# Kernel optimization log

Measured on AMD Instinct MI355X. Metric: run time of the kernel, lower is better.

The kernel has to match this reference:

```python
import jax, jax.numpy as jnp
import numpy as np

N = 50000      # nodes
E = 1000000    # edges
D = 64         # hidden dim
F_IN = 19      # node feature dim (nfeat_node)
EH = 50        # edge attr dim (nc_edge_hidden)
B = 128        # graphs in batch
NB = 3         # n_block
CUTOFF = 5.0
LOG2 = 0.6931471805599453


def ssp(x):
    # shifted softplus, Act('ssp')
    return jax.nn.softplus(x) - LOG2


def setup_inputs() -> dict:
    key = jax.random.key(0)
    ks = iter(jax.random.split(key, 48))
    def nrm(shape, scale=0.05):
        return jax.random.normal(next(ks), shape, dtype=jnp.float32) * scale
    inp = {}
    inp['x'] = jax.random.normal(next(ks), (N, F_IN), dtype=jnp.float32)
    inp['edge_index'] = jax.random.randint(next(ks), (2, E), 0, N)
    inp['edge_weight'] = jax.random.uniform(next(ks), (E,), dtype=jnp.float32, minval=0.5, maxval=CUTOFF)
    inp['edge_attr'] = jax.random.normal(next(ks), (E, EH), dtype=jnp.float32)
    inp['z'] = jax.random.randint(next(ks), (N,), 0, 100)
    inp['batch'] = jnp.sort(jax.random.randint(next(ks), (N,), 0, B))
    inp['lin0_w'] = nrm((D, F_IN)); inp['lin0_b'] = nrm((D,))
    # 3 NNConv blocks, weights stacked on leading axis
    inp['conv_mlp_w1'] = nrm((NB, 32, EH)); inp['conv_mlp_b1'] = nrm((NB, 32))
    inp['conv_mlp_w2'] = nrm((NB, D, 32)); inp['conv_mlp_b2'] = nrm((NB, D))
    inp['conv_lin1_w'] = nrm((NB, D, D))
    inp['conv_lin2_w'] = nrm((NB, D, D)); inp['conv_lin2_b'] = nrm((NB, D))
    inp['conv_lin3_w'] = nrm((NB, D, D)); inp['conv_lin3_b'] = nrm((NB, D))
    inp['gru_w_ih'] = nrm((3 * D, D)); inp['gru_w_hh'] = nrm((3 * D, D))
    inp['gru_b_ih'] = nrm((3 * D,)); inp['gru_b_hh'] = nrm((3 * D,))
    # Set2Set LSTM: input 2*D, hidden D
    inp['lstm_w_ih'] = nrm((4 * D, 2 * D)); inp['lstm_w_hh'] = nrm((4 * D, D))
    inp['lstm_b_ih'] = nrm((4 * D,)); inp['lstm_b_hh'] = nrm((4 * D,))
    inp['lin1_w'] = nrm((D, 2 * D)); inp['lin1_b'] = nrm((D,))
    inp['lin2_w'] = nrm((1, D)); inp['lin2_b'] = nrm((1,))
    inp['atom_ref'] = nrm((100, 1)); inp['energy_ref'] = nrm((100, 1))
    return inp


def _forward(x, edge_weight, edge_attr, lin0_w, lin0_b,
             conv_mlp_w1, conv_mlp_b1, conv_mlp_w2, conv_mlp_b2,
             conv_lin1_w, conv_lin2_w, conv_lin2_b, conv_lin3_w, conv_lin3_b,
             gru_w_ih, gru_w_hh, gru_b_ih, gru_b_hh,
             lstm_w_ih, lstm_w_hh, lstm_b_ih, lstm_b_hh,
             lin1_w, lin1_b, lin2_w, lin2_b, atom_ref, energy_ref,
             edge_index, z, batch):
    src = edge_index[0]   # neighbor j (source)
    dst = edge_index[1]   # center i (target), aggr='mean'
    deg = jnp.clip(jax.ops.segment_sum(jnp.ones((E,), jnp.float32), dst, num_segments=N), 1.0, None)
    # cosine cutoff envelope
    C = jnp.cos(edge_weight * jnp.pi / CUTOFF) * 0.5 + 0.5  # (E,)
    out = jax.nn.leaky_relu(x @ lin0_w.T + lin0_b)  # (N, D)
    h = out
    for b in range(NB):
        # edge MLP: Linear(EH,32) -> ReLU -> Linear(32,D), scaled by envelope
        Wm = jax.nn.relu(edge_attr @ conv_mlp_w1[b].T + conv_mlp_b1[b]) @ conv_mlp_w2[b].T + conv_mlp_b2[b]
        Wm = Wm * C[:, None]  # (E, D)
        hx = out @ conv_lin1_w[b].T  # (N, D)
        msg = hx[src] * Wm  # gather + per-edge product  (E, D)
        agg = jax.ops.segment_sum(msg, dst, num_segments=N) / deg[:, None]  # mean aggregation
        m = ssp(agg @ conv_lin2_w[b].T + conv_lin2_b[b]) @ conv_lin3_w[b].T + conv_lin3_b[b]
        # GRU node-state update (single step)
        gi = m @ gru_w_ih.T + gru_b_ih
        gh = h @ gru_w_hh.T + gru_b_hh
        i_r, i_z, i_n = jnp.split(gi, 3, axis=-1)
        h_r, h_z, h_n = jnp.split(gh, 3, axis=-1)
        r = jax.nn.sigmoid(i_r + h_r)
        zg = jax.nn.sigmoid(i_z + h_z)
        n = jnp.tanh(i_n + r * h_n)
        h = (1.0 - zg) * n + zg * h
        out = h
    # Set2Set readout, processing_steps=3
    q_star = jnp.zeros((B, 2 * D), jnp.float32)
    hl = jnp.zeros((B, D), jnp.float32)
    cl = jnp.zeros((B, D), jnp.float32)
    for _ in range(3):
        gates = q_star @ lstm_w_ih.T + lstm_b_ih + hl @ lstm_w_hh.T + lstm_b_hh
        gi_, gf_, gg_, go_ = jnp.split(gates, 4, axis=-1)
        cl = jax.nn.sigmoid(gf_) * cl + jax.nn.sigmoid(gi_) * jnp.tanh(gg_)
        hl = jax.nn.sigmoid(go_) * jnp.tanh(cl)
        q = hl  # (B, D)
        e = jnp.sum(out * q[batch], axis=-1)  # (N,)
        emax = jax.ops.segment_max(e, batch, num_segments=B)
        a = jnp.exp(e - emax[batch])
        asum = jax.ops.segment_sum(a, batch, num_segments=B)
        a = a / asum[batch]  # per-graph softmax attention
        r_read = jax.ops.segment_sum(a[:, None] * out, batch, num_segments=B)
        q_star = jnp.concatenate([q, r_read], axis=-1)
    g = jax.nn.relu(q_star @ lin1_w.T + lin1_b)
    energy = g @ lin2_w.T + lin2_b  # (B, 1)
    ref = jax.ops.segment_sum((energy_ref[z] + atom_ref[z])[:, 0], batch, num_segments=B)
    return energy + ref[:, None]


def reference(x, edge_weight, edge_attr, lin0_w, lin0_b,
              conv_mlp_w1, conv_mlp_b1, conv_mlp_w2, conv_mlp_b2,
              conv_lin1_w, conv_lin2_w, conv_lin2_b, conv_lin3_w, conv_lin3_b,
              gru_w_ih, gru_w_hh, gru_b_ih, gru_b_hh,
              lstm_w_ih, lstm_w_hh, lstm_b_ih, lstm_b_hh,
              lin1_w, lin1_b, lin2_w, lin2_b, atom_ref, energy_ref,
              edge_index, z, batch):
    return _forward(x, edge_weight, edge_attr, lin0_w, lin0_b,
                    conv_mlp_w1, conv_mlp_b1, conv_mlp_w2, conv_mlp_b2,
                    conv_lin1_w, conv_lin2_w, conv_lin2_b, conv_lin3_w, conv_lin3_b,
                    gru_w_ih, gru_w_hh, gru_b_ih, gru_b_hh,
                    lstm_w_ih, lstm_w_hh, lstm_b_ih, lstm_b_hh,
                    lin1_w, lin1_b, lin2_w, lin2_b, atom_ref, energy_ref,
                    edge_index, z, batch)
```

## Files before the change

kernel.cpp:

```cpp
#include <hip/hip_runtime.h>
#include <math.h>

#define NN 50000
#define NE 1000000
#define D 64
#define FIN 19
#define EHD 50
#define NG 128
#define NBLK 3
#define NB1 196
#define EAPW 32

#define PI_OVER_CUT 0.6283185307179586f
#define LN2F 0.6931471805599453f

static __device__ __forceinline__ float sspf(float x) {
  return fmaxf(x, 0.0f) + log1pf(expf(-fabsf(x))) - LN2F;
}
static __device__ __forceinline__ float sigm(float x) {
  return 1.0f / (1.0f + expf(-x));
}

typedef _Float16 h2f __attribute__((ext_vector_type(2)));
typedef __fp16   p2f __attribute__((ext_vector_type(2)));
typedef unsigned int u32x4 __attribute__((ext_vector_type(4)));

static __device__ __forceinline__ unsigned int f16pair(float a, float b) {
  p2f r = __builtin_amdgcn_cvt_pkrtz(a, b);
  return __builtin_bit_cast(unsigned int, r);
}
static __device__ __forceinline__ float f16lo(unsigned int u) {
  h2f v = __builtin_bit_cast(h2f, u);
  return (float)v.x;
}
static __device__ __forceinline__ float f16hi(unsigned int u) {
  h2f v = __builtin_bit_cast(h2f, u);
  return (float)v.y;
}

#if __has_builtin(__builtin_amdgcn_fdot2)
static __device__ __forceinline__ float dot2(unsigned int a, unsigned int b, float c) {
  return __builtin_amdgcn_fdot2(__builtin_bit_cast(h2f, a),
                                __builtin_bit_cast(h2f, b), c, false);
}
#else
static __device__ __forceinline__ float dot2(unsigned int a, unsigned int b, float c) {
  h2f a2 = __builtin_bit_cast(h2f, a), b2 = __builtin_bit_cast(h2f, b);
  return c + (float)a2.x * (float)b2.x + (float)a2.y * (float)b2.y;
}
#endif

__global__ __launch_bounds__(256) void k_deg(const int* __restrict__ ei,
                                             int* __restrict__ degi) {
  int e = blockIdx.x * 256 + threadIdx.x;
  if (e < NE) atomicAdd(&degi[ei[NE + e]], 1);
}

__global__ __launch_bounds__(256) void k_scan1(int* __restrict__ degi,
                                               int* __restrict__ start,
                                               float* __restrict__ dinv,
                                               int* __restrict__ bsum) {
  __shared__ int sc[256];
  int t = threadIdx.x;
  int i = blockIdx.x * 256 + t;
  int d = (i < NN) ? degi[i] : 0;
  sc[t] = d; __syncthreads();
  for (int off = 1; off < 256; off <<= 1) {
    int u = (t >= off) ? sc[t - off] : 0;
    __syncthreads();
    sc[t] += u;
    __syncthreads();
  }
  if (i < NN) {
    start[i] = sc[t] - d;
    dinv[i] = 1.0f / fmaxf((float)d, 1.0f);
    degi[i] = 0;
  }
  if (t == 255) bsum[blockIdx.x] = sc[255];
}

__global__ __launch_bounds__(256) void k_scan2(int* __restrict__ bsum) {
  __shared__ int sc[256];
  int t = threadIdx.x;
  int v = (t < NB1) ? bsum[t] : 0;
  sc[t] = v; __syncthreads();
  for (int off = 1; off < 256; off <<= 1) {
    int u = (t >= off) ? sc[t - off] : 0;
    __syncthreads();
    sc[t] += u;
    __syncthreads();
  }
  bsum[t] = sc[t] - v;
}

__global__ __launch_bounds__(256) void k_scan3(int* __restrict__ start,
                                               const int* __restrict__ bsum) {
  int i = blockIdx.x * 256 + threadIdx.x;
  if (i < NN) start[i] += bsum[blockIdx.x];
  if (i == 0) start[NN] = NE;
}

template<int PACK>
__global__ __launch_bounds__(256) void k_slot2(const int* __restrict__ ei,
                                               const int* __restrict__ start,
                                               int* __restrict__ cursor,
                                               int* __restrict__ es,
                                               const float* __restrict__ ea,
                                               unsigned int* __restrict__ eap) {
  int e = blockIdx.x * 256 + threadIdx.x;
  if (e >= NE) return;
  int dst = ei[NE + e];
  int ofs = atomicAdd(&cursor[dst], 1);
  int s = start[dst] + ofs;
  es[s] = e;
  if (PACK) {
    const float2* er = (const float2*)(ea + (size_t)e * EHD);
    unsigned int tmp[25];
    #pragma unroll
    for (int k2 = 0; k2 < 25; k2++) {
      float2 v = er[k2];
      tmp[k2] = f16pair(v.x, v.y);
    }
    u32x4* op = (u32x4*)(eap + (size_t)s * EAPW);
    #pragma unroll
    for (int i = 0; i < 6; i++) {
      u32x4 v4 = {tmp[4*i], tmp[4*i+1], tmp[4*i+2], tmp[4*i+3]};
      __builtin_nontemporal_store(v4, op + i);
    }
    u32x4 v6 = {tmp[24], 0u, 0u, 0u};
    __builtin_nontemporal_store(v6, op + 6);
    u32x4 v7 = {0u, 0u, 0u, 0u};
    __builtin_nontemporal_store(v7, op + 7);
  }
}

__global__ __launch_bounds__(256) void k_fill(const int* __restrict__ es,
                                              const int* __restrict__ ei,
                                              const float* __restrict__ ew,
                                              int* __restrict__ ssrc,
                                              int* __restrict__ sdst,
                                              float* __restrict__ Cp) {
  int s = blockIdx.x * 256 + threadIdx.x;
  if (s >= NE) return;
  int e = es[s];
  ssrc[s] = ei[e];
  sdst[s] = ei[NE + e];
  Cp[s] = cosf(ew[e] * PI_OVER_CUT) * 0.5f + 0.5f;
}

__global__ __launch_bounds__(256) void k_wprep(const float* __restrict__ w1,
                                               const float* __restrict__ w2,
                                               const float* __restrict__ cl2w,
                                               const float* __restrict__ cl3w,
                                               const float* __restrict__ cl1w,
                                               const float* __restrict__ gwih,
                                               const float* __restrict__ gwhh,
                                               unsigned int* __restrict__ w1h,
                                               unsigned int* __restrict__ w2h,
                                               unsigned int* __restrict__ nl2h,
                                               unsigned int* __restrict__ nl3h,
                                               unsigned int* __restrict__ nl1h,
                                               unsigned int* __restrict__ gih,
                                               unsigned int* __restrict__ ghh) {
  int i = blockIdx.x * 256 + threadIdx.x;
  if (i < 2400) {
    int b = i / 800, r = i % 800, j = r / 25, k2 = r % 25;
    const float* src = w1 + ((size_t)(b * 32 + j) * EHD + 2 * k2);
    w1h[i] = f16pair(src[0], src[1]);
    return;
  }
  int i2 = i - 2400;
  if (i2 < 3072) {
    int b = i2 / 1024, r = i2 % 1024, d = r / 16, p = r % 16;
    const float* src = w2 + ((size_t)(b * 64 + d) * 32 + 2 * p);
    w2h[i2] = f16pair(src[0], src[1]);
    return;
  }
  int i3 = i2 - 3072;
  if (i3 < 3 * 6144) {
    int which = i3 / 6144, j3 = i3 % 6144;
    int b = j3 / 2048, r = j3 % 2048, d = r / 32, kp = r % 32;
    const float* W = (which == 0) ? cl2w : (which == 1) ? cl3w : cl1w;
    unsigned int* O = (which == 0) ? nl2h : (which == 1) ? nl3h : nl1h;
    const float* src = W + (size_t)b * 4096 + d * 64 + 2 * kp;
    O[j3] = f16pair(src[0], src[1]);
    return;
  }
  int i4 = i3 - 3 * 6144;
  if (i4 < 2 * 6144) {
    int which = i4 / 6144, j4 = i4 % 6144;
    int row = j4 / 32, kp = j4 % 32;
    const float* W = which ? gwhh : gwih;
    unsigned int* O = which ? ghh : gih;
    const float* src = W + (size_t)row * 64 + 2 * kp;
    O[j4] = f16pair(src[0], src[1]);
  }
}

__global__ void k_bounds(const int* __restrict__ batch, int* __restrict__ bounds) {
  int g = threadIdx.x;
  if (g > NG) return;
  int lo = 0, hi = NN;
  while (lo < hi) { int mid = (lo + hi) >> 1; if (batch[mid] < g) lo = mid + 1; else hi = mid; }
  bounds[g] = lo;
}

__global__ __launch_bounds__(256) void k_lin0q(const float* __restrict__ x,
                                               const float* __restrict__ w,
                                               const float* __restrict__ bias,
                                               float* __restrict__ S) {
  int n = blockIdx.x * 256 + threadIdx.x;
  int q = blockIdx.y;
  if (n >= NN) return;
  float xr[FIN];
  #pragma unroll
  for (int k = 0; k < FIN; k++) xr[k] = x[n * FIN + k];
  #pragma unroll
  for (int i = 0; i < 16; i++) {
    int d = q * 16 + i;
    float a0 = bias[d], a1 = 0.f;
    #pragma unroll
    for (int k = 0; k < FIN - 1; k += 2) {
      a0 += xr[k] * w[d * FIN + k];
      a1 += xr[k + 1] * w[d * FIN + k + 1];
    }
    a0 += xr[FIN - 1] * w[d * FIN + FIN - 1];
    float acc = a0 + a1;
    S[(size_t)n * D + d] = acc > 0.f ? acc : 0.01f * acc;
  }
}

__global__ __launch_bounds__(256) void k_hx0(const float* __restrict__ in,
                                             const float* __restrict__ w,
                                             unsigned int* __restrict__ hxh) {
  __shared__ float tile[64 * 65];
  int tid = threadIdx.x;
  long nb = (long)blockIdx.x * 64;
  const float4* src = (const float4*)(in + nb * D);
  #pragma unroll
  for (int r = 0; r < 4; r++) {
    int idx = r * 256 + tid;
    int row = idx >> 4, c4 = idx & 15;
    float4 v = src[idx];
    float* dp = &tile[row * 65 + c4 * 4];
    dp[0] = v.x; dp[1] = v.y; dp[2] = v.z; dp[3] = v.w;
  }
  __syncthreads();
  int q = __builtin_amdgcn_readfirstlane(tid >> 6);
  int lane = tid & 63;
  float acc[16];
  const float* wr = w + q * 16 * D;
  #pragma unroll
  for (int i = 0; i < 16; i++) acc[i] = 0.0f;
  for (int k = 0; k < D; k++) {
    float a = tile[lane * 65 + k];
    #pragma unroll
    for (int i = 0; i < 16; i++) acc[i] += a * wr[i * D + k];
  }
  if (nb + lane < NN) {
    uint2* out = (uint2*)(hxh + (size_t)(nb + lane) * 32);
    #pragma unroll
    for (int i = 0; i < 4; i++)
      out[q * 4 + i] = make_uint2(f16pair(acc[4*i], acc[4*i+1]),
                                  f16pair(acc[4*i+2], acc[4*i+3]));
  }
}

template<int SRC>
__global__ __launch_bounds__(256) void k_econv4(const float* __restrict__ ea,
                                                const unsigned int* __restrict__ eap,
                                                const int* __restrict__ es,
                                                const float* __restrict__ w1,
                                                const unsigned int* __restrict__ w1h,
                                                const float* __restrict__ b1,
                                                const unsigned int* __restrict__ w2h,
                                                const float* __restrict__ b2,
                                                const float* __restrict__ Cp,
                                                const int* __restrict__ ssrc,
                                                const int* __restrict__ sdst,
                                                const unsigned int* __restrict__ hxh,
                                                float* __restrict__ agg) {
  __shared__ float tileAll[4 * 16 * 68];
  int tid = threadIdx.x;
  int wid = tid >> 6, lane = tid & 63;
  float* tile = tileAll + wid * (16 * 68);
  int s = blockIdx.x * 256 + tid;
  if (s >= NE) return;
  int srcn = ssrc[s];
  int me = sdst[s];
  float cv = Cp[s];
  int pm = __shfl_up(me, 1);
  bool bound = (lane == 0) || (me != pm);
  unsigned long long segmask = __ballot(bound);
  unsigned int t1h[16];
  if (SRC == 1) {
    const uint4* ep4 = (const uint4*)(eap + (size_t)s * EAPW);
    uint4 q0 = ep4[0], q1 = ep4[1], q2 = ep4[2], q3 = ep4[3], q4 = ep4[4],
          q5 = ep4[5];
    unsigned int q6 = ((const unsigned int*)(ep4 + 6))[0];
    unsigned int arrh[25] = {q0.x, q0.y, q0.z, q0.w, q1.x, q1.y, q1.z, q1.w,
                             q2.x, q2.y, q2.z, q2.w, q3.x, q3.y, q3.z, q3.w,
                             q4.x, q4.y, q4.z, q4.w, q5.x, q5.y, q5.z, q5.w,
                             q6};
    float t1[32];
    #pragma unroll
    for (int j = 0; j < 32; j++) {
      float acc = b1[j];
      #pragma unroll
      for (int k = 0; k < 25; k++) acc = dot2(arrh[k], w1h[j * 25 + k], acc);
      t1[j] = fmaxf(acc, 0.0f);
    }
    #pragma unroll
    for (int p = 0; p < 16; p++) t1h[p] = f16pair(t1[2 * p], t1[2 * p + 1]);
  } else {
    int e = es[s];
    float arr[EHD];
    const float2* er = (const float2*)(ea + (size_t)e * EHD);
    #pragma unroll
    for (int k2 = 0; k2 < EHD / 2; k2++) {
      float2 v = er[k2];
      arr[2 * k2] = v.x; arr[2 * k2 + 1] = v.y;
    }
    float t1[32];
    #pragma unroll
    for (int j = 0; j < 32; j++) {
      float a0 = b1[j], a1 = 0.f;
      #pragma unroll
      for (int k = 0; k < EHD; k += 2) {
        a0 += arr[k]     * w1[j * EHD + k];
        a1 += arr[k + 1] * w1[j * EHD + k + 1];
      }
      t1[j] = fmaxf(a0 + a1, 0.0f);
    }
    #pragma unroll
    for (int p = 0; p < 16; p++) t1h[p] = f16pair(t1[2 * p], t1[2 * p + 1]);
  }
  const uint4* hrow4 = (const uint4*)(hxh + (size_t)srcn * 32);
  int dim = lane >> 2, r = lane & 3;
  #pragma unroll
  for (int c = 0; c < 4; c++) {
    uint4 ha = hrow4[c * 2], hb = hrow4[c * 2 + 1];
    unsigned int pw[8] = {ha.x, ha.y, ha.z, ha.w, hb.x, hb.y, hb.z, hb.w};
    float mg[16];
    #pragma unroll
    for (int u = 0; u < 16; u++) {
      int d = c * 16 + u;
      float acc = b2[d];
      #pragma unroll
      for (int p = 0; p < 16; p++) acc = dot2(t1h[p], w2h[d * 16 + p], acc);
      float hc = (u & 1) ? f16hi(pw[u >> 1]) : f16lo(pw[u >> 1]);
      mg[u] = acc * cv * hc;
    }
    #pragma unroll
    for (int u = 0; u < 16; u++) tile[u * 68 + lane] = mg[u];
    asm volatile("s_waitcnt lgkmcnt(0)" ::: "memory");
    unsigned long long mask = segmask;
    while (mask) {
      int l0 = __ffsll((unsigned long long)mask) - 1;
      unsigned long long rest = mask & (mask - 1);
      int l1 = rest ? (__ffsll((unsigned long long)rest) - 1) : 64;
      mask = rest;
      int node = __shfl(me, l0);
      float v = 0.f;
      for (int sl = l0 + r; sl < l1; sl += 4)
        v += tile[dim * 68 + sl];
      v += __shfl_xor(v, 1);
      v += __shfl_xor(v, 2);
      if (r == 0)
        atomicAdd(&agg[(size_t)node * D + c * 16 + dim], v);
    }
    asm volatile("s_waitcnt lgkmcnt(0)" ::: "memory");
  }
}

__global__ __launch_bounds__(256) void k_nodeblk(const float* __restrict__ agg,
                                                 const float* __restrict__ dinv,
                                                 const float* __restrict__ hin,
                                                 const unsigned int* __restrict__ w2h,
                                                 const float* __restrict__ b2,
                                                 const unsigned int* __restrict__ w3h,
                                                 const float* __restrict__ b3,
                                                 const unsigned int* __restrict__ gih,
                                                 const unsigned int* __restrict__ ghh,
                                                 const float* __restrict__ bih,
                                                 const float* __restrict__ bhh,
                                                 float* __restrict__ hout,
                                                 const unsigned int* __restrict__ w1nh,
                                                 unsigned int* __restrict__ hxout) {
  __shared__ unsigned int tA[64 * 33];
  __shared__ unsigned int tH[64 * 33];
  __shared__ float tS[64 * 65];
  int tid = threadIdx.x;
  long nb = (long)blockIdx.x * 64;
  const float4* as = (const float4*)(agg + nb * D);
  const float4* hs = (const float4*)(hin + nb * D);
  #pragma unroll
  for (int r = 0; r < 4; r++) {
    int idx = r * 256 + tid;
    int row = idx >> 4, c4 = idx & 15;
    float dv = dinv[nb + row];
    float4 v = as[idx];
    tA[row * 33 + 2 * c4]     = f16pair(v.x * dv, v.y * dv);
    tA[row * 33 + 2 * c4 + 1] = f16pair(v.z * dv, v.w * dv);
    float4 u = hs[idx];
    tH[row * 33 + 2 * c4]     = f16pair(u.x, u.y);
    tH[row * 33 + 2 * c4 + 1] = f16pair(u.z, u.w);
  }
  __syncthreads();
  int q = __builtin_amdgcn_readfirstlane(tid >> 6);
  int lane = tid & 63;
  {
    float acc[16];
    const unsigned int* wr = w2h + q * 16 * 32;
    #pragma unroll
    for (int i = 0; i < 16; i++) acc[i] = b2[q * 16 + i];
    for (int kp = 0; kp < 32; kp++) {
      unsigned int a = tA[lane * 33 + kp];
      #pragma unroll
      for (int i = 0; i < 16; i++) acc[i] = dot2(a, wr[i * 32 + kp], acc[i]);
    }
    __syncthreads();
    #pragma unroll
    for (int i = 0; i < 8; i++)
      tA[lane * 33 + q * 8 + i] = f16pair(sspf(acc[2 * i]), sspf(acc[2 * i + 1]));
    __syncthreads();
  }
  {
    float acc[16];
    const unsigned int* wr = w3h + q * 16 * 32;
    #pragma unroll
    for (int i = 0; i < 16; i++) acc[i] = b3[q * 16 + i];
    for (int kp = 0; kp < 32; kp++) {
      unsigned int a = tA[lane * 33 + kp];
      #pragma unroll
      for (int i = 0; i < 16; i++) acc[i] = dot2(a, wr[i * 32 + kp], acc[i]);
    }
    __syncthreads();
    #pragma unroll
    for (int i = 0; i < 8; i++)
      tA[lane * 33 + q * 8 + i] = f16pair(acc[2 * i], acc[2 * i + 1]);
    __syncthreads();
  }
  {
    float ir[16], iz[16], inn[16], hr[16], hz[16], hn[16];
    #pragma unroll
    for (int i = 0; i < 16; i++) {
      int dd = q * 16 + i;
      ir[i] = bih[dd]; iz[i] = bih[D + dd]; inn[i] = bih[2 * D + dd];
      hr[i] = bhh[dd]; hz[i] = bhh[D + dd]; hn[i] = bhh[2 * D + dd];
    }
    const unsigned int* wi0 = gih + (q * 16) * 32;
    const unsigned int* wi1 = gih + (64 + q * 16) * 32;
    const unsigned int* wi2 = gih + (128 + q * 16) * 32;
    const unsigned int* wh0 = ghh + (q * 16) * 32;
    const unsigned int* wh1 = ghh + (64 + q * 16) * 32;
    const unsigned int* wh2 = ghh + (128 + q * 16) * 32;
    for (int kp = 0; kp < 32; kp++) {
      unsigned int mm = tA[lane * 33 + kp];
      unsigned int hh = tH[lane * 33 + kp];
      #pragma unroll
      for (int i = 0; i < 16; i++) {
        ir[i]  = dot2(mm, wi0[i * 32 + kp], ir[i]);
        iz[i]  = dot2(mm, wi1[i * 32 + kp], iz[i]);
        inn[i] = dot2(mm, wi2[i * 32 + kp], inn[i]);
        hr[i]  = dot2(hh, wh0[i * 32 + kp], hr[i]);
        hz[i]  = dot2(hh, wh1[i * 32 + kp], hz[i]);
        hn[i]  = dot2(hh, wh2[i * 32 + kp], hn[i]);
      }
    }
    __syncthreads();
    float hv_[16];
    #pragma unroll
    for (int i = 0; i < 16; i++) {
      unsigned int hw = tH[lane * 33 + q * 8 + (i >> 1)];
      float hold = (i & 1) ? f16hi(hw) : f16lo(hw);
      float r_ = sigm(ir[i] + hr[i]);
      float zg = sigm(iz[i] + hz[i]);
      float nn2 = tanhf(inn[i] + r_ * hn[i]);
      hv_[i] = (1.0f - zg) * nn2 + zg * hold;
      tS[lane * 65 + q * 16 + i] = hv_[i];
    }
    #pragma unroll
    for (int i = 0; i < 8; i++)
      tA[lane * 33 + q * 8 + i] = f16pair(hv_[2 * i], hv_[2 * i + 1]);
    __syncthreads();
  }
  float4* dst = (float4*)(hout + nb * D);
  #pragma unroll
  for (int r = 0; r < 4; r++) {
    int idx = r * 256 + tid;
    int row = idx >> 4, c4 = idx & 15;
    if (nb + row < NN) {
      const float* sp = &tS[row * 65 + c4 * 4];
      dst[idx] = make_float4(sp[0], sp[1], sp[2], sp[3]);
    }
  }
  if (w1nh) {
    float acc[16];
    const unsigned int* wr = w1nh + q * 16 * 32;
    #pragma unroll
    for (int i = 0; i < 16; i++) acc[i] = 0.0f;
    for (int kp = 0; kp < 32; kp++) {
      unsigned int a = tA[lane * 33 + kp];
      #pragma unroll
      for (int i = 0; i < 16; i++) acc[i] = dot2(a, wr[i * 32 + kp], acc[i]);
    }
    if (nb + lane < NN) {
      uint2* out = (uint2*)(hxout + (size_t)(nb + lane) * 32);
      #pragma unroll
      for (int i = 0; i < 4; i++)
        out[q * 4 + i] = make_uint2(f16pair(acc[4*i], acc[4*i+1]),
                                    f16pair(acc[4*i+2], acc[4*i+3]));
    }
  }
}

__global__ __launch_bounds__(256) void k_s2s(const float* __restrict__ wih,
                                             const float* __restrict__ whh,
                                             const float* __restrict__ bih,
                                             const float* __restrict__ bhh,
                                             const float* __restrict__ S,
                                             const int* __restrict__ bounds,
                                             float* __restrict__ qstar,
                                             float* __restrict__ hl,
                                             float* __restrict__ cl,
                                             float* __restrict__ ebuf) {
  __shared__ float qv[D];
  __shared__ float red[256];
  int g = blockIdx.x, tid = threadIdx.x;
  if (tid < D) {
    int d = tid;
    const float* qs = qstar + g * 2 * D;
    const float* hr = hl + g * D;
    float ai = bih[d]         + bhh[d];
    float af = bih[D + d]     + bhh[D + d];
    float ag = bih[2 * D + d] + bhh[2 * D + d];
    float ao = bih[3 * D + d] + bhh[3 * D + d];
    #pragma unroll 8
    for (int k = 0; k < 2 * D; k++) {
      float q = qs[k];
      ai += q * wih[d * 2 * D + k];
      af += q * wih[(D + d) * 2 * D + k];
      ag += q * wih[(2 * D + d) * 2 * D + k];
      ao += q * wih[(3 * D + d) * 2 * D + k];
    }
    #pragma unroll 8
    for (int k = 0; k < D; k++) {
      float h = hr[k];
      ai += h * whh[d * D + k];
      af += h * whh[(D + d) * D + k];
      ag += h * whh[(2 * D + d) * D + k];
      ao += h * whh[(3 * D + d) * D + k];
    }
    float c = sigm(af) * cl[g * D + d] + sigm(ai) * tanhf(ag);
    float hn = sigm(ao) * tanhf(c);
    cl[g * D + d] = c;
    hl[g * D + d] = hn;
    qstar[g * 2 * D + d] = hn;
    qv[d] = hn;
  }
  __syncthreads();
  int s = bounds[g], en = bounds[g + 1];
  float lmax = -1e30f;
  for (int n = s + tid; n < en; n += 256) {
    const float4* Sv = (const float4*)(S + (size_t)n * D);
    float a0 = 0, a1 = 0, a2 = 0, a3 = 0;
    #pragma unroll
    for (int q = 0; q < 16; q++) {
      float4 v = Sv[q];
      a0 += v.x * qv[4*q]; a1 += v.y * qv[4*q+1];
      a2 += v.z * qv[4*q+2]; a3 += v.w * qv[4*q+3];
    }
    float e = (a0 + a1) + (a2 + a3);
    ebuf[n] = e;
    lmax = fmaxf(lmax, e);
  }
  red[tid] = lmax; __syncthreads();
  for (int st = 128; st > 0; st >>= 1) {
    if (tid < st) red[tid] = fmaxf(red[tid], red[tid + st]);
    __syncthreads();
  }
  float smax = red[0]; __syncthreads();
  float lsum = 0;
  for (int n = s + tid; n < en; n += 256) {
    float p = expf(ebuf[n] - smax);
    ebuf[n] = p;
    lsum += p;
  }
  red[tid] = lsum; __syncthreads();
  for (int st = 128; st > 0; st >>= 1) {
    if (tid < st) red[tid] += red[tid + st];
    __syncthreads();
  }
  float inv = red[0] > 0.f ? 1.0f / red[0] : 0.0f;
  __syncthreads();
  int grp = tid >> 6, d = tid & 63;
  float acc = 0;
  for (int n = s + grp; n < en; n += 4)
    acc += ebuf[n] * S[(size_t)n * D + d];
  red[tid] = acc; __syncthreads();
  if (tid < D)
    qstar[g * 2 * D + D + tid] =
        (red[tid] + red[64 + tid] + red[128 + tid] + red[192 + tid]) * inv;
}

__global__ __launch_bounds__(64) void k_final(const float* __restrict__ qstar,
                                              const float* __restrict__ w1,
                                              const float* __restrict__ b1,
                                              const float* __restrict__ w2,
                                              const float* __restrict__ b2,
                                              const int* __restrict__ z,
                                              const float* __restrict__ eref,
                                              const float* __restrict__ aref,
                                              const int* __restrict__ bounds,
                                              float* __restrict__ outp) {
  __shared__ float red[D];
  int g = blockIdx.x, d = threadIdx.x;
  const float* qs = qstar + g * 2 * D;
  float a0 = 0, a1 = 0, a2 = 0, a3 = 0;
  #pragma unroll
  for (int k = 0; k < 2 * D; k += 4) {
    a0 += qs[k]   * w1[d * 2 * D + k];
    a1 += qs[k+1] * w1[d * 2 * D + k + 1];
    a2 += qs[k+2] * w1[d * 2 * D + k + 2];
    a3 += qs[k+3] * w1[d * 2 * D + k + 3];
  }
  float gv = fmaxf((a0 + a1) + (a2 + a3) + b1[d], 0.0f);
  red[d] = gv * w2[d];
  __syncthreads();
  for (int st = 32; st > 0; st >>= 1) {
    if (d < st) red[d] += red[d + st];
    __syncthreads();
  }
  float energy = red[0] + b2[0];
  __syncthreads();
  int s = bounds[g], en = bounds[g + 1];
  float racc = 0;
  for (int n = s + d; n < en; n += 64) {
    int zz = z[n];
    racc += eref[zz] + aref[zz];
  }
  red[d] = racc; __syncthreads();
  for (int st = 32; st > 0; st >>= 1) {
    if (d < st) red[d] += red[d + st];
    __syncthreads();
  }
  if (d == 0) outp[g] = energy + red[0];
}

extern "C" void kernel_launch(void* const* d_in, const int* in_sizes, int n_in,
                              void* d_out, int out_size, void* d_ws, size_t ws_size,
                              hipStream_t stream) {
  const float* x      = (const float*)d_in[0];
  const int*   ei     = (const int*)d_in[1];
  const float* ew     = (const float*)d_in[2];
  const float* ea     = (const float*)d_in[3];
  const int*   z      = (const int*)d_in[4];
  const int*   batch  = (const int*)d_in[5];
  const float* lin0_w = (const float*)d_in[6];
  const float* lin0_b = (const float*)d_in[7];
  const float* cw1    = (const float*)d_in[8];
  const float* cb1    = (const float*)d_in[9];
  const float* cw2    = (const float*)d_in[10];
  const float* cb2    = (const float*)d_in[11];
  const float* cl1w   = (const float*)d_in[12];
  const float* cl2w   = (const float*)d_in[13];
  const float* cl2b   = (const float*)d_in[14];
  const float* cl3w   = (const float*)d_in[15];
  const float* cl3b   = (const float*)d_in[16];
  const float* gwih   = (const float*)d_in[17];
  const float* gwhh   = (const float*)d_in[18];
  const float* gbih   = (const float*)d_in[19];
  const float* gbhh   = (const float*)d_in[20];
  const float* lwih   = (const float*)d_in[21];
  const float* lwhh   = (const float*)d_in[22];
  const float* lbih   = (const float*)d_in[23];
  const float* lbhh   = (const float*)d_in[24];
  const float* l1w    = (const float*)d_in[25];
  const float* l1b    = (const float*)d_in[26];
  const float* l2w    = (const float*)d_in[27];
  const float* l2b    = (const float*)d_in[28];
  const float* aref   = (const float*)d_in[29];
  const float* eref   = (const float*)d_in[30];
  float* outp = (float*)d_out;

  const long NND = (long)NN * D;
  float* f = (float*)d_ws;
  long cur = 0;
  long oS0 = cur;   cur += NND;
  long oS1 = cur;   cur += NND;
  long oHX = cur;   cur += 1600000;
  long oAG = cur;   cur += NND;
  long oCP = cur;   cur += NE;
  long oDI = cur;   cur += 50176;
  long oEB = cur;   cur += 50176;
  long oQ  = cur;   cur += NG * 2 * D;
  long oHL = cur;   cur += NG * D;
  long oCL = cur;   cur += NG * D;
  long oBN = cur;   cur += 256;
  long oES = cur;   cur += NE;
  long oSR = cur;   cur += NE;
  long oSD = cur;   cur += NE;
  long oST = cur;   cur += 51200;
  long oBS = cur;   cur += 256;
  long oW1H = cur;  cur += 2432;
  long oW2H = cur;  cur += 3072;
  long oNL2 = cur;  cur += 6144;
  long oNL3 = cur;  cur += 6144;
  long oNL1 = cur;  cur += 6144;
  long oGIH = cur;  cur += 6144;
  long oGHH = cur;  cur += 6144;
  cur = (cur + 31) & ~31L;
  long baseEnd = cur;

  float* S0   = f + oS0;
  float* S1   = f + oS1;
  unsigned int* hxh = (unsigned int*)(f + oHX);
  float* aggb = f + oAG;
  float* Cp   = f + oCP;
  float* dinv = f + oDI;
  float* ebuf = f + oEB;
  int*   degi = (int*)(f + oEB);
  float* qstar= f + oQ;
  float* hl   = f + oHL;
  float* cls  = f + oCL;
  int*   bounds = (int*)(f + oBN);
  int*   es   = (int*)(f + oES);
  int*   ssrc = (int*)(f + oSR);
  int*   sdst = (int*)(f + oSD);
  int*   startA = (int*)(f + oST);
  int*   bsum = (int*)(f + oBS);
  unsigned int* w1h  = (unsigned int*)(f + oW1H);
  unsigned int* w2h  = (unsigned int*)(f + oW2H);
  unsigned int* nl2h = (unsigned int*)(f + oNL2);
  unsigned int* nl3h = (unsigned int*)(f + oNL3);
  unsigned int* nl1h = (unsigned int*)(f + oNL1);
  unsigned int* gih  = (unsigned int*)(f + oGIH);
  unsigned int* ghh  = (unsigned int*)(f + oGHH);

  long wsF = (long)(ws_size / 4);
  int useEap = (baseEnd + (long)NE * EAPW <= wsF) ? 1 : 0;
  unsigned int* eap = (unsigned int*)(f + baseEnd);

  hipMemsetAsync(degi, 0, NN * sizeof(int), stream);
  hipMemsetAsync(qstar, 0, (NG * 2 * D + 2 * NG * D) * sizeof(float), stream);

  k_deg<<<(NE + 255) / 256, 256, 0, stream>>>(ei, degi);
  k_scan1<<<NB1, 256, 0, stream>>>(degi, startA, dinv, bsum);
  k_scan2<<<1, 256, 0, stream>>>(bsum);
  k_scan3<<<NB1, 256, 0, stream>>>(startA, bsum);
  if (useEap)
    k_slot2<1><<<(NE + 255) / 256, 256, 0, stream>>>(ei, startA, degi, es, ea, eap);
  else
    k_slot2<0><<<(NE + 255) / 256, 256, 0, stream>>>(ei, startA, degi, es, ea, eap);
  k_fill<<<(NE + 255) / 256, 256, 0, stream>>>(es, ei, ew, ssrc, sdst, Cp);
  k_wprep<<<142, 256, 0, stream>>>(cw1, cw2, cl2w, cl3w, cl1w, gwih, gwhh,
                                   w1h, w2h, nl2h, nl3h, nl1h, gih, ghh);
  k_lin0q<<<dim3((NN + 255) / 256, 4), 256, 0, stream>>>(x, lin0_w, lin0_b, S0);
  k_bounds<<<1, 192, 0, stream>>>(batch, bounds);

  const int NBK = (NN + 63) / 64;
  k_hx0<<<NBK, 256, 0, stream>>>(S0, cl1w, hxh);

  for (int b = 0; b < NBLK; b++) {
    float* Sin  = (b & 1) ? S1 : S0;
    float* Sout = (b & 1) ? S0 : S1;
    hipMemsetAsync(aggb, 0, NND * sizeof(float), stream);
    if (useEap)
      k_econv4<1><<<(NE + 255) / 256, 256, 0, stream>>>(
          ea, eap, es, cw1 + b * 32 * EHD, w1h + b * 800, cb1 + b * 32,
          w2h + b * 1024, cb2 + b * D, Cp, ssrc, sdst, hxh, aggb);
    else
      k_econv4<0><<<(NE + 255) / 256, 256, 0, stream>>>(
          ea, eap, es, cw1 + b * 32 * EHD, w1h + b * 800, cb1 + b * 32,
          w2h + b * 1024, cb2 + b * D, Cp, ssrc, sdst, hxh, aggb);
    const unsigned int* w1nh = (b + 1 < NBLK) ? (nl1h + (b + 1) * 2048) : nullptr;
    k_nodeblk<<<NBK, 256, 0, stream>>>(aggb, dinv, Sin,
                                       nl2h + b * 2048, cl2b + b * D,
                                       nl3h + b * 2048, cl3b + b * D,
                                       gih, ghh, gbih, gbhh,
                                       Sout, w1nh, hxh);
  }

  float* Sfin = (NBLK & 1) ? S1 : S0;
  for (int it = 0; it < 3; it++) {
    k_s2s<<<NG, 256, 0, stream>>>(lwih, lwhh, lbih, lbhh, Sfin, bounds,
                                  qstar, hl, cls, ebuf);
  }

  k_final<<<NG, 64, 0, stream>>>(qstar, l1w, l1b, l2w, l2b, z, eref, aref,
                                 bounds, outp);
}
```

Measured before the change: 1.064 ms.

## Pack edge attributes in original edge order with separate coalesced kernel

Moves the fp16 packing of edge attributes out of the scatter kernel into a dedicated kernel that writes the packed array in original edge order, one element per thread with coalesced reads and writes. The scatter kernel no longer does strided per-thread reads and scattered 128-byte writes. In exchange, the three edge-conv passes now gather packed attributes through the sorted-to-original index (es), so their reads become random instead of sequential.

```diff
diff --git a/kernel.cpp b/kernel.cpp
--- a/kernel.cpp
+++ b/kernel.cpp
@@ -23,7 +23,6 @@
 
 typedef _Float16 h2f __attribute__((ext_vector_type(2)));
 typedef __fp16   p2f __attribute__((ext_vector_type(2)));
-typedef unsigned int u32x4 __attribute__((ext_vector_type(4)));
 
 static __device__ __forceinline__ unsigned int f16pair(float a, float b) {
   p2f r = __builtin_amdgcn_cvt_pkrtz(a, b);
@@ -100,38 +99,29 @@
   if (i == 0) start[NN] = NE;
 }
 
-template<int PACK>
 __global__ __launch_bounds__(256) void k_slot2(const int* __restrict__ ei,
                                                const int* __restrict__ start,
                                                int* __restrict__ cursor,
-                                               int* __restrict__ es,
-                                               const float* __restrict__ ea,
-                                               unsigned int* __restrict__ eap) {
+                                               int* __restrict__ es) {
   int e = blockIdx.x * 256 + threadIdx.x;
   if (e >= NE) return;
   int dst = ei[NE + e];
   int ofs = atomicAdd(&cursor[dst], 1);
-  int s = start[dst] + ofs;
-  es[s] = e;
-  if (PACK) {
-    const float2* er = (const float2*)(ea + (size_t)e * EHD);
-    unsigned int tmp[25];
-    #pragma unroll
-    for (int k2 = 0; k2 < 25; k2++) {
-      float2 v = er[k2];
-      tmp[k2] = f16pair(v.x, v.y);
-    }
-    u32x4* op = (u32x4*)(eap + (size_t)s * EAPW);
-    #pragma unroll
-    for (int i = 0; i < 6; i++) {
-      u32x4 v4 = {tmp[4*i], tmp[4*i+1], tmp[4*i+2], tmp[4*i+3]};
-      __builtin_nontemporal_store(v4, op + i);
-    }
-    u32x4 v6 = {tmp[24], 0u, 0u, 0u};
-    __builtin_nontemporal_store(v6, op + 6);
-    u32x4 v7 = {0u, 0u, 0u, 0u};
-    __builtin_nontemporal_store(v7, op + 7);
-  }
+  es[start[dst] + ofs] = e;
+}
+
+__global__ __launch_bounds__(256) void k_pack(const float* __restrict__ ea,
+                                              unsigned int* __restrict__ eap) {
+  long o = (long)blockIdx.x * 256 + threadIdx.x;
+  if (o >= (long)NE * EAPW) return;
+  long e = o >> 5;
+  int k = (int)(o & 31);
+  unsigned int v = 0u;
+  if (k < 25) {
+    const float* p = ea + e * EHD + 2 * k;
+    v = f16pair(p[0], p[1]);
+  }
+  eap[o] = v;
 }
 
 __global__ __launch_bounds__(256) void k_fill(const int* __restrict__ es,
@@ -286,6 +276,7 @@
   float* tile = tileAll + wid * (16 * 68);
   int s = blockIdx.x * 256 + tid;
   if (s >= NE) return;
+  int e = es[s];
   int srcn = ssrc[s];
   int me = sdst[s];
   float cv = Cp[s];
@@ -294,7 +285,7 @@
   unsigned long long segmask = __ballot(bound);
   unsigned int t1h[16];
   if (SRC == 1) {
-    const uint4* ep4 = (const uint4*)(eap + (size_t)s * EAPW);
+    const uint4* ep4 = (const uint4*)(eap + (size_t)e * EAPW);
     uint4 q0 = ep4[0], q1 = ep4[1], q2 = ep4[2], q3 = ep4[3], q4 = ep4[4],
           q5 = ep4[5];
     unsigned int q6 = ((const unsigned int*)(ep4 + 6))[0];
@@ -313,7 +304,6 @@
     #pragma unroll
     for (int p = 0; p < 16; p++) t1h[p] = f16pair(t1[2 * p], t1[2 * p + 1]);
   } else {
-    int e = es[s];
     float arr[EHD];
     const float2* er = (const float2*)(ea + (size_t)e * EHD);
     #pragma unroll
@@ -749,11 +739,10 @@
   k_scan1<<<NB1, 256, 0, stream>>>(degi, startA, dinv, bsum);
   k_scan2<<<1, 256, 0, stream>>>(bsum);
   k_scan3<<<NB1, 256, 0, stream>>>(startA, bsum);
+  k_slot2<<<(NE + 255) / 256, 256, 0, stream>>>(ei, startA, degi, es);
+  k_fill<<<(NE + 255) / 256, 256, 0, stream>>>(es, ei, ew, ssrc, sdst, Cp);
   if (useEap)
-    k_slot2<1><<<(NE + 255) / 256, 256, 0, stream>>>(ei, startA, degi, es, ea, eap);
-  else
-    k_slot2<0><<<(NE + 255) / 256, 256, 0, stream>>>(ei, startA, degi, es, ea, eap);
-  k_fill<<<(NE + 255) / 256, 256, 0, stream>>>(es, ei, ew, ssrc, sdst, Cp);
+    k_pack<<<(int)(((long)NE * EAPW + 255) / 256), 256, 0, stream>>>(ea, eap);
   k_wprep<<<142, 256, 0, stream>>>(cw1, cw2, cl2w, cl3w, cl1w, gwih, gwhh,
                                    w1h, w2h, nl2h, nl3h, nl1h, gih, ghh);
   k_lin0q<<<dim3((NN + 255) / 256, 4), 256, 0, stream>>>(x, lin0_w, lin0_b, S0);
```

Result: faster. 977.9 us (-8.1%).
